# Kernel tuning notes

Measured on AMD Instinct MI355X. Metric: run time of the kernel, lower is better.

Reference implementation:

```python
import jax, jax.numpy as jnp
import numpy as np
from jax import lax

N_SUBNETS = 4
NUM_BLOCK = 4
NUM_FEATURE = 64
SCALE = 2
SUBNET_BS = [768, 768, 768, 768]
H = W = 32
CLS_CH = 16


def conv2d(x, w, b):
    # x: [B,C,H,W], w: [O,I,3,3] SAME padding
    y = lax.conv_general_dilated(x, w, (1, 1), 'SAME',
                                 dimension_numbers=('NCHW', 'OIHW', 'NCHW'))
    return y + b[None, :, None, None]


def pixel_shuffle(x, s):
    # [B, C*s*s, H, W] -> [B, C, H*s, W*s]
    B, Cs, h, w = x.shape
    C = Cs // (s * s)
    x = x.reshape(B, C, s, s, h, w)
    x = x.transpose(0, 1, 4, 2, 5, 3)
    return x.reshape(B, C, h * s, w * s)


def setup_inputs() -> dict:
    key = jax.random.key(0)
    ks = jax.random.split(key, 16)
    F, E, Bk, s = NUM_FEATURE, N_SUBNETS, NUM_BLOCK, SCALE
    sc = lambda *shape: 0.05
    inp = {
        'inputs': jax.random.normal(ks[0], (2048, 3, H, W), jnp.float32),
        # classifier: conv3x3 3->16, relu, global avg pool, fc 16->E
        'cls_w1': jax.random.normal(ks[1], (CLS_CH, 3, 3, 3), jnp.float32) * 0.1,
        'cls_b1': jnp.zeros((CLS_CH,), jnp.float32),
        'cls_wfc': jax.random.normal(ks[2], (E, CLS_CH), jnp.float32) * 0.1,
        'cls_bfc': jnp.zeros((E,), jnp.float32),
        # per-expert SR subnet params (stacked over expert dim E)
        'head_w': jax.random.normal(ks[3], (E, F, 3, 3, 3), jnp.float32) * 0.1,
        'head_b': jnp.zeros((E, F), jnp.float32),
        'body_w': jax.random.normal(ks[4], (E, Bk, F, F, 3, 3), jnp.float32) * 0.05,
        'body_b': jnp.zeros((E, Bk, F), jnp.float32),
        'tail_w': jax.random.normal(ks[5], (E, 3 * s * s, F, 3, 3), jnp.float32) * 0.1,
        'tail_b': jnp.zeros((E, 3 * s * s), jnp.float32),
    }
    return inp


def _forward(inputs, cls_w1, cls_b1, cls_wfc, cls_bfc,
             head_w, head_b, body_w, body_b, tail_w, tail_b):
    N = inputs.shape[0]
    Ho, Wo = H * SCALE, W * SCALE
    # classifier scores [N, E]
    f = jax.nn.relu(conv2d(inputs, cls_w1, cls_b1))
    scores = jnp.mean(f, axis=(2, 3)) @ cls_wfc.T + cls_bfc
    expert = jnp.argmax(scores, axis=-1)  # top-1 scatter routing

    out = jnp.zeros((N, 3, Ho, Wo), inputs.dtype)
    for i in range(N_SUBNETS):
        cap = SUBNET_BS[i]
        mask = expert == i
        rank = jnp.cumsum(mask) - 1          # within-expert position
        valid = mask & (rank < cap)
        slot = jnp.where(valid, rank, cap)   # overflow/other -> dummy row
        # dispatch + pad to fixed capacity (resize_ to subnet_bs)
        buf = jnp.zeros((cap + 1, 3, H, W), inputs.dtype).at[slot].set(inputs)
        x = buf[:cap]
        # subnet: head conv -> num_block residual relu-convs -> tail + pixel shuffle
        h0 = conv2d(x, head_w[i], head_b[i])
        h = h0
        for b in range(NUM_BLOCK):
            h = jax.nn.relu(conv2d(h, body_w[i, b], body_b[i, b]))
        h = h + h0
        y = pixel_shuffle(conv2d(h, tail_w[i], tail_b[i]), SCALE)  # [cap,3,Ho,Wo]
        # unpad to real_bs and gather-combine back to original order
        y_ext = jnp.concatenate([y, jnp.zeros((1, 3, Ho, Wo), y.dtype)], axis=0)
        out = out + y_ext[slot] * valid[:, None, None, None].astype(y.dtype)
    return out


def reference(inputs, cls_w1, cls_b1, cls_wfc, cls_bfc,
              head_w, head_b, body_w, body_b, tail_w, tail_b):
    return _forward(inputs, cls_w1, cls_b1, cls_wfc, cls_bfc,
                    head_w, head_b, body_w, body_b, tail_w, tail_b)
```

## Files before the change

### kernel.cpp

```cpp
#include <hip/hip_runtime.h>
#include <hip/hip_bf16.h>

typedef unsigned short u16;
typedef short s8v __attribute__((ext_vector_type(8)));
typedef float f16v __attribute__((ext_vector_type(16)));

#define N_IMG   2048
#define F       64
#define EXPERTS 4
#define NBLK    4
#define CAP     768
#define CLS_CH  16
#define OUT_PER_IMG (3*64*64)

#define ACT_BYTES (1156*64*2)
#define IMG_OFF   ACT_BYTES
#define IMG_BYTES (1156*4*2)
#define LDS_BYTES (ACT_BYTES + IMG_BYTES)

#define SWZB(p, c) (((p) << 7) + ((c) ^ (((p) & 7) << 4)))

#define WS_EXPERT   0
#define WS_PERM     8192
#define WS_VLD      16384
#define WS_BODY     24576
#define WS_HEAD     (WS_BODY + 589824*2)
#define WS_TAIL     (WS_HEAD + 12288*2)

__device__ __forceinline__ u16 f2bf(float v) {
    return __builtin_bit_cast(u16, __float2bfloat16(v));
}
__device__ __forceinline__ unsigned pk2(float a, float b) {
    return (unsigned)f2bf(a) | ((unsigned)f2bf(b) << 16);
}

__global__ __launch_bounds__(256) void k_prep(
    const float* __restrict__ hw, const float* __restrict__ bw,
    const float* __restrict__ tw, u16* __restrict__ oh,
    u16* __restrict__ ob, u16* __restrict__ otl)
{
    const int i = blockIdx.x * 256 + threadIdx.x;
    if (i < 589824) {
        const int j = i & 7, lane = (i >> 3) & 63, ot = (i >> 9) & 1;
        const int kc = (i >> 10) & 3, tap = (i >> 12) % 9, lb = i / 36864;
        const int oc = ot*32 + (lane & 31);
        const int ci = kc*16 + (lane >> 5)*8 + j;
        ob[i] = f2bf(bw[((lb*64 + oc)*64 + ci)*9 + tap]);
    } else if (i < 589824 + 12288) {
        const int i2 = i - 589824;
        const int j = i2 & 7, lane = (i2 >> 3) & 63, ot = (i2 >> 9) & 1;
        const int kc = (i2 >> 10) % 3, e = i2 / 3072;
        const int oc = ot*32 + (lane & 31);
        const int k = kc*16 + (lane >> 5)*8 + j;
        const int tap = k >> 2, ci = k & 3;
        const float v = (k < 36 && ci < 3) ? hw[((e*64 + oc)*3 + ci)*9 + tap] : 0.f;
        oh[i2] = f2bf(v);
    } else if (i < 589824 + 12288 + 73728) {
        const int i2 = i - 602112;
        const int j = i2 & 7, lane = (i2 >> 3) & 63;
        const int kc = (i2 >> 9) & 3, tap = (i2 >> 11) % 9, e = i2 / 18432;
        const int oc = lane & 31;
        const int ci = kc*16 + (lane >> 5)*8 + j;
        const float v = (oc < 12) ? tw[((e*12 + oc)*64 + ci)*9 + tap] : 0.f;
        otl[i2] = f2bf(v);
    }
}

__global__ __launch_bounds__(256) void k_classify(
    const float* __restrict__ inp, const float* __restrict__ w1,
    const float* __restrict__ b1, const float* __restrict__ wfc,
    const float* __restrict__ bfc, int* __restrict__ expert)
{
    __shared__ float img[3*1024];
    __shared__ float wred[4][CLS_CH];
    __shared__ float meanf[CLS_CH];
    const int n = blockIdx.x, t = threadIdx.x;
    const float* src = inp + (size_t)n*3072;
    {
        const float4* s4 = (const float4*)src;
        float4* d4 = (float4*)img;
        for (int i = t; i < 768; i += 256) d4[i] = s4[i];
    }
    __syncthreads();

    float sums[CLS_CH];
    #pragma unroll
    for (int c = 0; c < CLS_CH; ++c) sums[c] = 0.f;

    #pragma unroll
    for (int k4 = 0; k4 < 4; ++k4) {
        const int p = t + k4*256, y = p >> 5, x = p & 31;
        float v[27];
        #pragma unroll
        for (int ci = 0; ci < 3; ++ci)
            #pragma unroll
            for (int dy = 0; dy < 3; ++dy)
                #pragma unroll
                for (int dx = 0; dx < 3; ++dx) {
                    const int py = y + dy - 1, px = x + dx - 1;
                    v[ci*9 + dy*3 + dx] =
                        ((unsigned)py < 32u && (unsigned)px < 32u)
                            ? img[ci*1024 + py*32 + px] : 0.f;
                }
        for (int c = 0; c < CLS_CH; ++c) {
            float o = b1[c];
            #pragma unroll
            for (int k = 0; k < 27; ++k) o += w1[c*27 + k] * v[k];
            sums[c] += fmaxf(o, 0.f);
        }
    }

    #pragma unroll
    for (int c = 0; c < CLS_CH; ++c) {
        float s = sums[c];
        #pragma unroll
        for (int m = 32; m >= 1; m >>= 1) s += __shfl_xor(s, m);
        sums[c] = s;
    }
    const int lane = t & 63, wv = t >> 6;
    if (lane == 0)
        #pragma unroll
        for (int c = 0; c < CLS_CH; ++c) wred[wv][c] = sums[c];
    __syncthreads();
    if (t < CLS_CH)
        meanf[t] = (wred[0][t] + wred[1][t] + wred[2][t] + wred[3][t]) * (1.0f/1024.0f);
    __syncthreads();
    if (t == 0) {
        float best = -1e30f; int bi = 0;
        for (int e = 0; e < EXPERTS; ++e) {
            float sc = bfc[e];
            for (int cc = 0; cc < CLS_CH; ++cc) sc += wfc[e*CLS_CH + cc] * meanf[cc];
            if (sc > best) { best = sc; bi = e; }
        }
        expert[n] = bi;
    }
}

__global__ __launch_bounds__(256) void k_route(
    const int* __restrict__ expert, int* __restrict__ perm, int* __restrict__ vld)
{
    __shared__ int cnt[EXPERTS];
    __shared__ int vbase[EXPERTS], obase[EXPERTS];
    const int t = threadIdx.x;
    const int wv = t >> 6, lane = t & 63;

    int my = 0;
    for (int c = 0; c < N_IMG/64; ++c) {
        const int e = expert[c*64 + lane];
        const unsigned long long m = __ballot(e == wv);
        my += (int)__popcll(m);
    }
    if (lane == 0) cnt[wv] = my;
    __syncthreads();
    if (t == 0) {
        int vb = 0;
        for (int e = 0; e < EXPERTS; ++e) {
            vbase[e] = vb; vb += (cnt[e] < CAP ? cnt[e] : CAP);
        }
        int ob = vb;
        for (int e = 0; e < EXPERTS; ++e) {
            obase[e] = ob; ob += (cnt[e] > CAP ? cnt[e] - CAP : 0);
        }
    }
    __syncthreads();

    int base = 0;
    for (int c = 0; c < N_IMG/64; ++c) {
        const int n = c*64 + lane;
        const int e = expert[n];
        const unsigned long long m = __ballot(e == wv);
        if (e == wv) {
            const int rank = base + (int)__popcll(m & ((1ull << lane) - 1ull));
            int slot, v;
            if (rank < CAP) { slot = vbase[wv] + rank;       v = 1; }
            else            { slot = obase[wv] + rank - CAP; v = 0; }
            perm[slot] = n; vld[slot] = v;
        }
        base += (int)__popcll(m);
    }
}

__device__ __forceinline__ s8v ld_act(const char* actb, int p, int c) {
    return *reinterpret_cast<const s8v*>(actb + SWZB(p, c));
}
__device__ __forceinline__ s8v ld_w(const u16* w, int eoff) {
    return *reinterpret_cast<const s8v*>(w + eoff);
}

__device__ __forceinline__ void bias_init(f16v acc[2][4], const float* bp, int h) {
    #pragma unroll
    for (int ot = 0; ot < 2; ++ot)
        #pragma unroll
        for (int g = 0; g < 4; ++g) {
            const float4 bv = *reinterpret_cast<const float4*>(bp + ot*32 + g*8 + h*4);
            const float* b4 = (const float*)&bv;
            #pragma unroll
            for (int pt = 0; pt < 4; ++pt)
                #pragma unroll
                for (int i = 0; i < 4; ++i)
                    acc[ot][pt][g*4+i] = b4[i];
        }
}
__device__ __forceinline__ void bias_add(f16v acc[2][4], const float* bp, int h) {
    #pragma unroll
    for (int ot = 0; ot < 2; ++ot)
        #pragma unroll
        for (int g = 0; g < 4; ++g) {
            const float4 bv = *reinterpret_cast<const float4*>(bp + ot*32 + g*8 + h*4);
            const float* b4 = (const float*)&bv;
            #pragma unroll
            for (int pt = 0; pt < 4; ++pt)
                #pragma unroll
                for (int i = 0; i < 4; ++i)
                    acc[ot][pt][g*4+i] += b4[i];
        }
}

__device__ __forceinline__ void body_gemm(f16v acc[2][4], const char* actb,
                                          const u16* wb, int lane, int y0) {
    const int r31 = lane & 31, h = lane >> 5;
    #pragma unroll
    for (int kc = 0; kc < 4; ++kc) {
        const int coff = kc*32 + h*16;
        #pragma unroll
        for (int dx = 0; dx < 3; ++dx) {
            s8v ar[6];
            #pragma unroll
            for (int r = 0; r < 6; ++r)
                ar[r] = ld_act(actb, (y0 + r)*34 + r31 + dx, coff);
            #pragma unroll
            for (int dy = 0; dy < 3; ++dy) {
                const int woff = ((dy*3 + dx)*4 + kc)*1024 + lane*8;
                const s8v w0 = ld_w(wb, woff);
                const s8v w1 = ld_w(wb, woff + 512);
                #pragma unroll
                for (int pt = 0; pt < 4; ++pt) {
                    acc[0][pt] = __builtin_amdgcn_mfma_f32_32x32x16_bf16(w0, ar[dy+pt], acc[0][pt], 0,0,0);
                    acc[1][pt] = __builtin_amdgcn_mfma_f32_32x32x16_bf16(w1, ar[dy+pt], acc[1][pt], 0,0,0);
                }
            }
        }
    }
}

__device__ __forceinline__ void head_gemm(f16v acc[2][4], const char* imgb,
                                          const u16* hw, int lane, int y0) {
    const int r31 = lane & 31, h = lane >> 5;
    #pragma unroll
    for (int kc = 0; kc < 3; ++kc) {
        const s8v w0 = ld_w(hw, kc*1024 + lane*8);
        const s8v w1 = ld_w(hw, kc*1024 + 512 + lane*8);
        #pragma unroll
        for (int pt = 0; pt < 4; ++pt) {
            const int y = y0 + pt;
            const int tA = kc*4 + h*2, tB = tA + 1;
            const int pA = (tA <= 8) ? (y + tA/3)*34 + r31 + (tA % 3) : 0;
            const int pB = (tB <= 8) ? (y + tB/3)*34 + r31 + (tB % 3) : 0;
            const uint2 lo = *reinterpret_cast<const uint2*>(imgb + pA*8);
            const uint2 hi = *reinterpret_cast<const uint2*>(imgb + pB*8);
            uint4 tmp; tmp.x = lo.x; tmp.y = lo.y; tmp.z = hi.x; tmp.w = hi.y;
            const s8v bf = __builtin_bit_cast(s8v, tmp);
            acc[0][pt] = __builtin_amdgcn_mfma_f32_32x32x16_bf16(w0, bf, acc[0][pt], 0,0,0);
            acc[1][pt] = __builtin_amdgcn_mfma_f32_32x32x16_bf16(w1, bf, acc[1][pt], 0,0,0);
        }
    }
}

__device__ __forceinline__ void st_act(char* actb, const f16v acc[2][4],
                                       int r31, int h, int y0) {
    #pragma unroll
    for (int pt = 0; pt < 4; ++pt) {
        const int p = (y0 + pt + 1)*34 + r31 + 1;
        #pragma unroll
        for (int ot = 0; ot < 2; ++ot)
            #pragma unroll
            for (int g = 0; g < 4; ++g) {
                uint2 wv;
                wv.x = pk2(acc[ot][pt][g*4+0], acc[ot][pt][g*4+1]);
                wv.y = pk2(acc[ot][pt][g*4+2], acc[ot][pt][g*4+3]);
                *reinterpret_cast<uint2*>(actb + SWZB(p, ot*64 + g*16 + h*8)) = wv;
            }
    }
}

__global__ __launch_bounds__(512, 2) void k_sr(
    const float* __restrict__ inp,
    const float* __restrict__ head_b, const float* __restrict__ body_b,
    const float* __restrict__ tail_b,
    const u16* __restrict__ bw_head, const u16* __restrict__ bw_body,
    const u16* __restrict__ bw_tail,
    const int* __restrict__ perm, const int* __restrict__ vld,
    const int* __restrict__ expert, float* __restrict__ out)
{
    extern __shared__ char lds[];
    char* actb = lds;
    char* imgb = lds + IMG_OFF;
    const int slot = blockIdx.x, t = threadIdx.x;
    const int n = perm[slot];
    float* outp = out + (size_t)n * OUT_PER_IMG;

    if (!vld[slot]) {
        float4 z; z.x = z.y = z.z = z.w = 0.f;
        float4* o4 = (float4*)outp;
        #pragma unroll
        for (int k = 0; k < 6; ++k) o4[k*512 + t] = z;
        return;
    }
    const int e = expert[n];

    for (int i = t; i < LDS_BYTES/4; i += 512) ((unsigned*)lds)[i] = 0u;
    __syncthreads();

    const float* src = inp + (size_t)n*3072;
    #pragma unroll
    for (int k = 0; k < 6; ++k) {
        const int i = t + k*512;
        const int ci = i >> 10, p = i & 1023, y = p >> 5, x = p & 31;
        ((u16*)imgb)[((y+1)*34 + x + 1)*4 + ci] = f2bf(src[i]);
    }
    __syncthreads();

    const int lane = t & 63, wv = t >> 6;
    const int r31 = lane & 31, h = lane >> 5;
    const int y0 = wv * 4;

    const u16* hw = bw_head + e*3072;
    const float* hb = head_b + e*64;

    f16v acc[2][4];

    bias_init(acc, hb, h);
    head_gemm(acc, imgb, hw, lane, y0);
    st_act(actb, acc, r31, h, y0);
    __syncthreads();

    for (int b = 0; b < NBLK; ++b) {
        const u16* wb = bw_body + (size_t)(e*NBLK + b)*36864;
        bias_init(acc, body_b + (e*NBLK + b)*64, h);
        body_gemm(acc, actb, wb, lane, y0);
        #pragma unroll
        for (int ot = 0; ot < 2; ++ot)
            #pragma unroll
            for (int pt = 0; pt < 4; ++pt)
                #pragma unroll
                for (int i = 0; i < 16; ++i)
                    acc[ot][pt][i] = fmaxf(acc[ot][pt][i], 0.f);
        if (b == NBLK-1) {
            bias_add(acc, hb, h);
            head_gemm(acc, imgb, hw, lane, y0);
        }
        __syncthreads();
        st_act(actb, acc, r31, h, y0);
        __syncthreads();
    }

    {
        const u16* tw = bw_tail + e*18432;
        const float* tb = tail_b + e*12;
        f16v tacc[4];
        #pragma unroll
        for (int pt = 0; pt < 4; ++pt)
            #pragma unroll
            for (int g = 0; g < 4; ++g)
                #pragma unroll
                for (int i = 0; i < 4; ++i) {
                    const int tc = g*8 + h*4 + i;
                    tacc[pt][g*4+i] = (tc < 12) ? tb[tc] : 0.f;
                }
        #pragma unroll
        for (int kc = 0; kc < 4; ++kc) {
            const int coff = kc*32 + h*16;
            #pragma unroll
            for (int dx = 0; dx < 3; ++dx) {
                s8v ar[6];
                #pragma unroll
                for (int r = 0; r < 6; ++r)
                    ar[r] = ld_act(actb, (y0 + r)*34 + r31 + dx, coff);
                #pragma unroll
                for (int dy = 0; dy < 3; ++dy) {
                    const s8v twf = ld_w(tw, ((dy*3 + dx)*4 + kc)*512 + lane*8);
                    #pragma unroll
                    for (int pt = 0; pt < 4; ++pt)
                        tacc[pt] = __builtin_amdgcn_mfma_f32_32x32x16_bf16(twf, ar[dy+pt], tacc[pt], 0,0,0);
                }
            }
        }
        #pragma unroll
        for (int pt = 0; pt < 4; ++pt) {
            const int ys = y0 + pt;
            #pragma unroll
            for (int g = 0; g < 2; ++g)
                #pragma unroll
                for (int i2 = 0; i2 < 2; ++i2) {
                    const int tc0 = g*8 + h*4 + i2*2;
                    if (tc0 < 12) {
                        const int co = tc0 >> 2;
                        const int yo = 2*ys + ((tc0 >> 1) & 1);
                        float2 v2;
                        v2.x = tacc[pt][g*4 + i2*2];
                        v2.y = tacc[pt][g*4 + i2*2 + 1];
                        *reinterpret_cast<float2*>(&outp[co*4096 + yo*64 + 2*r31]) = v2;
                    }
                }
        }
    }
}

extern "C" void kernel_launch(void* const* d_in, const int* in_sizes, int n_in,
                              void* d_out, int out_size, void* d_ws, size_t ws_size,
                              hipStream_t stream) {
    const float* inp     = (const float*)d_in[0];
    const float* cls_w1  = (const float*)d_in[1];
    const float* cls_b1  = (const float*)d_in[2];
    const float* cls_wfc = (const float*)d_in[3];
    const float* cls_bfc = (const float*)d_in[4];
    const float* head_w  = (const float*)d_in[5];
    const float* head_b  = (const float*)d_in[6];
    const float* body_w  = (const float*)d_in[7];
    const float* body_b  = (const float*)d_in[8];
    const float* tail_w  = (const float*)d_in[9];
    const float* tail_b  = (const float*)d_in[10];
    float* out = (float*)d_out;

    char* ws = (char*)d_ws;
    int* expert = (int*)(ws + WS_EXPERT);
    int* perm   = (int*)(ws + WS_PERM);
    int* vld    = (int*)(ws + WS_VLD);
    u16* bw_body = (u16*)(ws + WS_BODY);
    u16* bw_head = (u16*)(ws + WS_HEAD);
    u16* bw_tail = (u16*)(ws + WS_TAIL);

    hipFuncSetAttribute((const void*)k_sr,
                        hipFuncAttributeMaxDynamicSharedMemorySize, LDS_BYTES);

    k_prep<<<(675840 + 255)/256, 256, 0, stream>>>(head_w, body_w, tail_w,
                                                   bw_head, bw_body, bw_tail);
    k_classify<<<N_IMG, 256, 0, stream>>>(inp, cls_w1, cls_b1, cls_wfc, cls_bfc, expert);
    k_route<<<1, 256, 0, stream>>>(expert, perm, vld);
    k_sr<<<N_IMG, 512, LDS_BYTES, stream>>>(inp, head_b, body_b, tail_b,
                                            bw_head, bw_body, bw_tail,
                                            perm, vld, expert, out);
}
```

Baseline: 574.2 us.

## Double-buffer body GEMM operand loads, raise MFMA priority, use nontemporal output stores

Restructures the body convolution GEMM into a flattened 12-step loop that prefetches the next step's activation and weight fragments into a second register buffer while the current MFMAs run. The MFMA sections in the body and tail are wrapped in s_setprio so matrix work gets issue priority over other waves. Output writes, including zero-fill for invalid slots, become nontemporal stores to avoid polluting cache. The change costs registers from the doubled operand buffers, which could cause spills under the 512-thread, 2-block launch bound.

```diff
diff --git a/kernel.cpp b/kernel.cpp
--- a/kernel.cpp
+++ b/kernel.cpp
@@ -32,6 +32,11 @@
 }
 __device__ __forceinline__ unsigned pk2(float a, float b) {
     return (unsigned)f2bf(a) | ((unsigned)f2bf(b) << 16);
+}
+__device__ __forceinline__ void nt_store2(float* p, float a, float b) {
+    float2 v; v.x = a; v.y = b;
+    __builtin_nontemporal_store(__builtin_bit_cast(unsigned long long, v),
+                                (unsigned long long*)p);
 }
 
 __global__ __launch_bounds__(256) void k_prep(
@@ -219,27 +224,45 @@
 __device__ __forceinline__ void body_gemm(f16v acc[2][4], const char* actb,
                                           const u16* wb, int lane, int y0) {
     const int r31 = lane & 31, h = lane >> 5;
-    #pragma unroll
-    for (int kc = 0; kc < 4; ++kc) {
-        const int coff = kc*32 + h*16;
-        #pragma unroll
-        for (int dx = 0; dx < 3; ++dx) {
-            s8v ar[6];
+    s8v ar[2][6], wA[2][3], wB[2][3];
+
+    {
+        const int coff = h*16;
+        #pragma unroll
+        for (int r = 0; r < 6; ++r)
+            ar[0][r] = ld_act(actb, (y0 + r)*34 + r31, coff);
+        #pragma unroll
+        for (int dy = 0; dy < 3; ++dy) {
+            const int woff = (dy*3)*4096 + lane*8;
+            wA[0][dy] = ld_w(wb, woff);
+            wB[0][dy] = ld_w(wb, woff + 512);
+        }
+    }
+    #pragma unroll
+    for (int g = 0; g < 12; ++g) {
+        const int b  = g & 1, nb = b ^ 1;
+        if (g < 11) {
+            const int kn = (g+1)/3, dn = (g+1)%3;
+            const int coffn = kn*32 + h*16;
             #pragma unroll
             for (int r = 0; r < 6; ++r)
-                ar[r] = ld_act(actb, (y0 + r)*34 + r31 + dx, coff);
+                ar[nb][r] = ld_act(actb, (y0 + r)*34 + r31 + dn, coffn);
             #pragma unroll
             for (int dy = 0; dy < 3; ++dy) {
-                const int woff = ((dy*3 + dx)*4 + kc)*1024 + lane*8;
-                const s8v w0 = ld_w(wb, woff);
-                const s8v w1 = ld_w(wb, woff + 512);
-                #pragma unroll
-                for (int pt = 0; pt < 4; ++pt) {
-                    acc[0][pt] = __builtin_amdgcn_mfma_f32_32x32x16_bf16(w0, ar[dy+pt], acc[0][pt], 0,0,0);
-                    acc[1][pt] = __builtin_amdgcn_mfma_f32_32x32x16_bf16(w1, ar[dy+pt], acc[1][pt], 0,0,0);
-                }
+                const int woff = ((dy*3 + dn)*4 + kn)*1024 + lane*8;
+                wA[nb][dy] = ld_w(wb, woff);
+                wB[nb][dy] = ld_w(wb, woff + 512);
             }
         }
+        __builtin_amdgcn_s_setprio(1);
+        #pragma unroll
+        for (int dy = 0; dy < 3; ++dy)
+            #pragma unroll
+            for (int pt = 0; pt < 4; ++pt) {
+                acc[0][pt] = __builtin_amdgcn_mfma_f32_32x32x16_bf16(wA[b][dy], ar[b][dy+pt], acc[0][pt], 0,0,0);
+                acc[1][pt] = __builtin_amdgcn_mfma_f32_32x32x16_bf16(wB[b][dy], ar[b][dy+pt], acc[1][pt], 0,0,0);
+            }
+        __builtin_amdgcn_s_setprio(0);
     }
 }
 
@@ -300,10 +323,9 @@
     float* outp = out + (size_t)n * OUT_PER_IMG;
 
     if (!vld[slot]) {
-        float4 z; z.x = z.y = z.z = z.w = 0.f;
-        float4* o4 = (float4*)outp;
-        #pragma unroll
-        for (int k = 0; k < 6; ++k) o4[k*512 + t] = z;
+        #pragma unroll
+        for (int k = 0; k < 12; ++k)
+            nt_store2(outp + (k*512 + t)*2, 0.f, 0.f);
         return;
     }
     const int e = expert[n];
@@ -376,6 +398,7 @@
                 #pragma unroll
                 for (int r = 0; r < 6; ++r)
                     ar[r] = ld_act(actb, (y0 + r)*34 + r31 + dx, coff);
+                __builtin_amdgcn_s_setprio(1);
                 #pragma unroll
                 for (int dy = 0; dy < 3; ++dy) {
                     const s8v twf = ld_w(tw, ((dy*3 + dx)*4 + kc)*512 + lane*8);
@@ -383,6 +406,7 @@
                     for (int pt = 0; pt < 4; ++pt)
                         tacc[pt] = __builtin_amdgcn_mfma_f32_32x32x16_bf16(twf, ar[dy+pt], tacc[pt], 0,0,0);
                 }
+                __builtin_amdgcn_s_setprio(0);
             }
         }
         #pragma unroll
@@ -396,10 +420,8 @@
                     if (tc0 < 12) {
                         const int co = tc0 >> 2;
                         const int yo = 2*ys + ((tc0 >> 1) & 1);
-                        float2 v2;
-                        v2.x = tacc[pt][g*4 + i2*2];
-                        v2.y = tacc[pt][g*4 + i2*2 + 1];
-                        *reinterpret_cast<float2*>(&outp[co*4096 + yo*64 + 2*r31]) = v2;
+                        nt_store2(&outp[co*4096 + yo*64 + 2*r31],
+                                  tacc[pt][g*4 + i2*2], tacc[pt][g*4 + i2*2 + 1]);
                     }
                 }
         }
```

After: 662.3 us. 1.15x slower.
